# Kernel optimization log

Hardware: AMD Instinct MI355X
Metric: run time of the kernel (lower is better)

Reference implementation:

```python
import jax, jax.numpy as jnp
import numpy as np

T_STEPS = 4  # number of SNN timesteps

def zif(u):
    # Heaviside step (surrogate grad only matters for bwd)
    return (u >= 0).astype(u.dtype)

def setup_inputs() -> dict:
    key = jax.random.key(0)
    k1, = jax.random.split(key, 1)
    x = jax.random.normal(k1, (T_STEPS * 32, 256, 32, 32), dtype=jnp.float32)
    thresh = jnp.ones((), dtype=jnp.float32)
    return {"x": x, "thresh": thresh, "T": T_STEPS}

def reference(x, thresh, T):
    # Expand temporal dim: [T*B, C, H, W] -> [T, B, C, H, W]
    TB = x.shape[0]
    B = TB // T
    xt = x.reshape((T, B) + x.shape[1:])
    mem0 = jnp.broadcast_to(0.5 * thresh, xt.shape[1:]).astype(x.dtype)

    def step(mem, x_t):
        mem = mem + x_t
        spike = zif(mem - thresh) * thresh
        mem = mem - spike
        return mem, spike

    _, spikes = jax.lax.scan(step, mem0, xt)
    # Merge temporal dim back: [T, B, ...] -> [T*B, ...]
    return spikes.reshape((TB,) + x.shape[1:])
```

## Files before the change

### kernel.cpp

```cpp
#include <hip/hip_runtime.h>


#define T_STEPS 4
#define UNROLL 8
#define BLOCK 256

typedef float vfloat4 __attribute__((ext_vector_type(4)));

__global__ __launch_bounds__(256) void IF_18622978195596_kernel(
    const vfloat4* __restrict__ x, const float* __restrict__ thresh_p,
    vfloat4* __restrict__ out, int n4) {
    const int base = blockIdx.x * (BLOCK * UNROLL) + threadIdx.x;
    const float th = *thresh_p;

    const volatile vfloat4* __restrict__ xv_ptr = x;

    vfloat4 xv[UNROLL][T_STEPS];
#pragma unroll
    for (int u = 0; u < UNROLL; ++u) {
        const int i = base + u * BLOCK;
#pragma unroll
        for (int t = 0; t < T_STEPS; ++t) {
            xv[u][t] = xv_ptr[(size_t)t * n4 + i];
        }
    }
    __builtin_amdgcn_sched_barrier(0);

#pragma unroll
    for (int u = 0; u < UNROLL; ++u) {
        const int i = base + u * BLOCK;
        vfloat4 mem = {0.5f * th, 0.5f * th, 0.5f * th, 0.5f * th};
#pragma unroll
        for (int t = 0; t < T_STEPS; ++t) {
            mem += xv[u][t];
            vfloat4 s;
            s.x = (mem.x >= th) ? th : 0.0f;
            s.y = (mem.y >= th) ? th : 0.0f;
            s.z = (mem.z >= th) ? th : 0.0f;
            s.w = (mem.w >= th) ? th : 0.0f;
            mem -= s;
            __builtin_nontemporal_store(s, &out[(size_t)t * n4 + i]);
        }
    }
}

extern "C" void kernel_launch(void* const* d_in, const int* in_sizes, int n_in,
                              void* d_out, int out_size, void* d_ws,
                              size_t ws_size, hipStream_t stream) {
    const float* x = (const float*)d_in[0];
    const float* thresh = (const float*)d_in[1];
    float* out = (float*)d_out;

    int total = in_sizes[0];
    int n_per_t = total / T_STEPS;
    int n4 = n_per_t / 4;

    int block = BLOCK;
    int per_block = block * UNROLL;
    int grid = n4 / per_block;
    IF_18622978195596_kernel<<<grid, block, 0, stream>>>(
        (const vfloat4*)x, thresh, (vfloat4*)out, n4);
}
```

Baseline: 242.5 us.

## Stream inputs through LDS with a 3-deep async global_load_lds pipeline

Replaces the load-everything-then-compute register scheme with a triple-buffered LDS pipeline. Async global-to-LDS loads are issued per chunk and gated with hand-counted vmcnt waits, so loads for later chunks overlap the spike computation and stores of earlier ones. This lowers register pressure, which may raise occupancy. The cost is LDS traffic, fragile manual waitcnt accounting that mixes in the nontemporal stores, and a 16-byte global_load_lds that needs hardware support.

Result: faster. 237.4 us (-2.1%).

```diff
diff --git a/kernel.cpp b/kernel.cpp
--- a/kernel.cpp
+++ b/kernel.cpp
@@ -2,7 +2,8 @@
 
 
 #define T_STEPS 4
-#define UNROLL 8
+#define NB 8
+#define D 3
 #define BLOCK 256
 
 typedef float vfloat4 __attribute__((ext_vector_type(4)));
@@ -10,38 +11,62 @@
 __global__ __launch_bounds__(256) void IF_18622978195596_kernel(
     const vfloat4* __restrict__ x, const float* __restrict__ thresh_p,
     vfloat4* __restrict__ out, int n4) {
-    const int base = blockIdx.x * (BLOCK * UNROLL) + threadIdx.x;
+    __shared__ vfloat4 lds[D * 4 * T_STEPS * 64];
+
+    const int tid = threadIdx.x;
+    const int wave = __builtin_amdgcn_readfirstlane(tid >> 6);
+    const int lane = tid & 63;
+    const int base = blockIdx.x * (BLOCK * NB) + tid;
     const float th = *thresh_p;
 
-    const volatile vfloat4* __restrict__ xv_ptr = x;
+#define ISSUE(j)                                                             \
+    {                                                                        \
+        _Pragma("unroll")                                                    \
+        for (int t = 0; t < T_STEPS; ++t) {                                  \
+            const vfloat4* gp_ = &x[(size_t)t * n4 + base + (j) * BLOCK];    \
+            vfloat4* lp_ = &lds[((((j) % D) * 4 + wave) * T_STEPS + t) * 64];\
+            __builtin_amdgcn_global_load_lds(                                \
+                (const __attribute__((address_space(1))) void*)gp_,          \
+                (__attribute__((address_space(3))) void*)lp_, 16, 0, 0);     \
+        }                                                                    \
+        __builtin_amdgcn_sched_barrier(0);         \
+    }
 
-    vfloat4 xv[UNROLL][T_STEPS];
-#pragma unroll
-    for (int u = 0; u < UNROLL; ++u) {
-        const int i = base + u * BLOCK;
-#pragma unroll
-        for (int t = 0; t < T_STEPS; ++t) {
-            xv[u][t] = xv_ptr[(size_t)t * n4 + i];
-        }
+#define SPK(VT, t)                                                           \
+    mem += VT;                                                               \
+    s.x = (mem.x >= th) ? th : 0.0f;                                         \
+    s.y = (mem.y >= th) ? th : 0.0f;                                         \
+    s.z = (mem.z >= th) ? th : 0.0f;                                         \
+    s.w = (mem.w >= th) ? th : 0.0f;                                         \
+    mem -= s;                                                                \
+    __builtin_nontemporal_store(s, &out[(size_t)(t) * n4 + i_]);
+
+#define STEP(j, WSTR)                                                        \
+    {                                                                        \
+        asm volatile("s_waitcnt vmcnt(" WSTR ")" ::: "memory");              \
+        __builtin_amdgcn_sched_barrier(0);                                   \
+        const int sb_ = (((j) % D) * 4 + wave) * T_STEPS;                    \
+        vfloat4 v0 = lds[(sb_ + 0) * 64 + lane];                             \
+        vfloat4 v1 = lds[(sb_ + 1) * 64 + lane];                             \
+        vfloat4 v2 = lds[(sb_ + 2) * 64 + lane];                             \
+        vfloat4 v3 = lds[(sb_ + 3) * 64 + lane];                             \
+        asm volatile("s_waitcnt lgkmcnt(0)" ::: "memory");                   \
+        __builtin_amdgcn_sched_barrier(0);   \
+        if ((j) + D < NB) ISSUE((j) + D);                                    \
+        const int i_ = base + (j) * BLOCK;                                   \
+        vfloat4 mem = {0.5f * th, 0.5f * th, 0.5f * th, 0.5f * th};          \
+        vfloat4 s;                                                           \
+        SPK(v0, 0) SPK(v1, 1) SPK(v2, 2) SPK(v3, 3)                          \
     }
-    __builtin_amdgcn_sched_barrier(0);
 
-#pragma unroll
-    for (int u = 0; u < UNROLL; ++u) {
-        const int i = base + u * BLOCK;
-        vfloat4 mem = {0.5f * th, 0.5f * th, 0.5f * th, 0.5f * th};
-#pragma unroll
-        for (int t = 0; t < T_STEPS; ++t) {
-            mem += xv[u][t];
-            vfloat4 s;
-            s.x = (mem.x >= th) ? th : 0.0f;
-            s.y = (mem.y >= th) ? th : 0.0f;
-            s.z = (mem.z >= th) ? th : 0.0f;
-            s.w = (mem.w >= th) ? th : 0.0f;
-            mem -= s;
-            __builtin_nontemporal_store(s, &out[(size_t)t * n4 + i]);
-        }
-    }
+    ISSUE(0) ISSUE(1) ISSUE(2)
+
+    STEP(0, "8")  STEP(1, "12") STEP(2, "16") STEP(3, "20")
+    STEP(4, "20") STEP(5, "20") STEP(6, "16") STEP(7, "12")
+
+#undef ISSUE
+#undef SPK
+#undef STEP
 }
 
 extern "C" void kernel_launch(void* const* d_in, const int* in_sizes, int n_in,
@@ -55,9 +80,8 @@
     int n_per_t = total / T_STEPS;
     int n4 = n_per_t / 4;
 
-    int block = BLOCK;
-    int per_block = block * UNROLL;
+    int per_block = BLOCK * NB;
     int grid = n4 / per_block;
-    IF_18622978195596_kernel<<<grid, block, 0, stream>>>(
+    IF_18622978195596_kernel<<<grid, BLOCK, 0, stream>>>(
         (const vfloat4*)x, thresh, (vfloat4*)out, n4);
 }
```
